# Kernel tuning notes

Hardware: AMD Instinct MI355X
Metric: run time of the kernel (lower is better)

Reference implementation:

```python
import jax, jax.numpy as jnp
import numpy as np

V, BLK, D, H, L = 32000, 2048, 768, 12, 2
HD = D // H

def _ln(x, g, b, eps=1e-5):
    m = jnp.mean(x, axis=-1, keepdims=True)
    v = jnp.var(x, axis=-1, keepdims=True)
    return (x - m) * jax.lax.rsqrt(v + eps) * g + b

def setup_inputs() -> dict:
    key = jax.random.key(0)
    ks = jax.random.split(key, 16)
    s = 0.02
    return {
        "idx": jax.random.randint(ks[0], (2, 2048), 0, V, dtype=jnp.int32),
        "wte": jax.random.normal(ks[1], (V, D), jnp.float32) * s,
        "wpe": jax.random.normal(ks[2], (BLK, D), jnp.float32) * s,
        "ln1_g": jnp.ones((L, D), jnp.float32),
        "ln1_b": jnp.zeros((L, D), jnp.float32),
        "qkv_w": jax.random.normal(ks[3], (L, 3 * D, D), jnp.float32) * s,
        "qkv_b": jnp.zeros((L, 3 * D), jnp.float32),
        "proj_w": jax.random.normal(ks[4], (L, D, D), jnp.float32) * s,
        "proj_b": jnp.zeros((L, D), jnp.float32),
        "ln2_g": jnp.ones((L, D), jnp.float32),
        "ln2_b": jnp.zeros((L, D), jnp.float32),
        "fc_w": jax.random.normal(ks[5], (L, 4 * D, D), jnp.float32) * s,
        "fc_b": jnp.zeros((L, 4 * D), jnp.float32),
        "fc2_w": jax.random.normal(ks[6], (L, D, 4 * D), jnp.float32) * s,
        "fc2_b": jnp.zeros((L, D), jnp.float32),
        "lnf_g": jnp.ones((D,), jnp.float32),
        "lnf_b": jnp.zeros((D,), jnp.float32),
    }

def reference(idx, wte, wpe, ln1_g, ln1_b, qkv_w, qkv_b, proj_w, proj_b,
              ln2_g, ln2_b, fc_w, fc_b, fc2_w, fc2_b, lnf_g, lnf_b):
    B, T = idx.shape
    x = wte[idx] + wpe[:T][None, :, :]  # [B,T,D]
    causal = jnp.tril(jnp.ones((T, T), dtype=bool))
    scale = 1.0 / np.sqrt(HD)
    for l in range(L):
        h = _ln(x, ln1_g[l], ln1_b[l])
        qkv = h @ qkv_w[l].T + qkv_b[l]               # [B,T,3D]
        q, k, v = jnp.split(qkv, 3, axis=-1)
        q = q.reshape(B, T, H, HD).transpose(0, 2, 1, 3)
        k = k.reshape(B, T, H, HD).transpose(0, 2, 1, 3)
        v = v.reshape(B, T, H, HD).transpose(0, 2, 1, 3)
        att = jnp.einsum('bhqd,bhkd->bhqk', q, k) * scale
        att = jnp.where(causal, att, -jnp.inf)
        att = jax.nn.softmax(att, axis=-1)
        y = jnp.einsum('bhqk,bhkd->bhqd', att, v)
        y = y.transpose(0, 2, 1, 3).reshape(B, T, D)
        x = x + y @ proj_w[l].T + proj_b[l]
        h = _ln(x, ln2_g[l], ln2_b[l])
        h = jax.nn.gelu(h @ fc_w[l].T + fc_b[l], approximate=False)
        x = x + h @ fc2_w[l].T + fc2_b[l]
    x = _ln(x, lnf_g, lnf_b)
    logits = x @ wte.T  # tied lm_head, [B,T,V]
    return logits
```

## Files before the change

kernel.cpp:

```cpp
#include <hip/hip_runtime.h>
#include <hip/hip_bf16.h>
#include <math.h>

#define BB 2
#define TT 2048
#define DD 768
#define HH 12
#define NTOK (BB*TT)
#define VV 32000
#define NL 2

typedef __hip_bfloat16 bf16;
typedef __attribute__((ext_vector_type(8))) short bf16x8;
typedef __attribute__((ext_vector_type(4))) float f32x4;

typedef const __attribute__((address_space(1))) unsigned int* gas_u32;
typedef __attribute__((address_space(3))) unsigned int* las_u32;

__device__ __forceinline__ void gload16(const bf16* g, bf16* l) {
    __builtin_amdgcn_global_load_lds((gas_u32)g, (las_u32)l, 16, 0, 0);
}

__global__ void cast_f2b(const float* __restrict__ in, bf16* __restrict__ out, int n4) {
    int i = blockIdx.x * 256 + threadIdx.x;
    if (i >= n4) return;
    float4 v = reinterpret_cast<const float4*>(in)[i];
    out[i*4+0] = __float2bfloat16(v.x);
    out[i*4+1] = __float2bfloat16(v.y);
    out[i*4+2] = __float2bfloat16(v.z);
    out[i*4+3] = __float2bfloat16(v.w);
}

__global__ void embed_k(const int* __restrict__ idx, const float* __restrict__ wte,
                        const float* __restrict__ wpe, float* __restrict__ x) {
    int i = blockIdx.x * 256 + threadIdx.x;
    int n = i / (DD/4), d4 = i - n * (DD/4);
    int tok = idx[n];
    int t = n & (TT - 1);
    float4 a = reinterpret_cast<const float4*>(wte + (size_t)tok * DD)[d4];
    float4 p = reinterpret_cast<const float4*>(wpe + (size_t)t * DD)[d4];
    float4 r; r.x = a.x+p.x; r.y = a.y+p.y; r.z = a.z+p.z; r.w = a.w+p.w;
    reinterpret_cast<float4*>(x)[i] = r;
}

__global__ __launch_bounds__(256) void ln_k(const float* __restrict__ x,
                                            const float* __restrict__ g,
                                            const float* __restrict__ b,
                                            bf16* __restrict__ out) {
    int row = blockIdx.x;
    int tid = threadIdx.x;
    const float* xr = x + (size_t)row * DD;
    float v0 = xr[tid], v1 = xr[tid + 256], v2 = xr[tid + 512];
    float s = v0 + v1 + v2;
    float ss = v0*v0 + v1*v1 + v2*v2;
    #pragma unroll
    for (int d = 1; d < 64; d <<= 1) { s += __shfl_xor(s, d, 64); ss += __shfl_xor(ss, d, 64); }
    __shared__ float sh[8];
    int w = tid >> 6;
    if ((tid & 63) == 0) { sh[w] = s; sh[4 + w] = ss; }
    __syncthreads();
    s  = sh[0] + sh[1] + sh[2] + sh[3];
    ss = sh[4] + sh[5] + sh[6] + sh[7];
    float mean = s * (1.0f / DD);
    float var  = ss * (1.0f / DD) - mean * mean;
    float rstd = rsqrtf(var + 1e-5f);
    bf16* orow = out + (size_t)row * DD;
    orow[tid]       = __float2bfloat16((v0 - mean) * rstd * g[tid]       + b[tid]);
    orow[tid + 256] = __float2bfloat16((v1 - mean) * rstd * g[tid + 256] + b[tid + 256]);
    orow[tid + 512] = __float2bfloat16((v2 - mean) * rstd * g[tid + 512] + b[tid + 512]);
}

template<int EPI>
__global__ __launch_bounds__(256) void gemm_bt(
    const bf16* __restrict__ A, const bf16* __restrict__ W,
    const float* __restrict__ bias, const float* __restrict__ resid,
    void* __restrict__ outp, int O, int K)
{
    __shared__ bf16 As[128 * 32];
    __shared__ bf16 Bs[128 * 32];
    const int tid = threadIdx.x;
    const int lane = tid & 63;
    const int w = tid >> 6;
    const int wm = w >> 1, wn = w & 1;
    const int rowBase = blockIdx.y * 128, colBase = blockIdx.x * 128;

    const int rr = lane & 15, kq = (lane >> 4) * 8;
    const int srow = lane >> 2;
    const int scol = (lane & 3) * 8;

    f32x4 acc[4][4];
    #pragma unroll
    for (int m = 0; m < 4; ++m)
        #pragma unroll
        for (int n = 0; n < 4; ++n) acc[m][n] = (f32x4){0.f, 0.f, 0.f, 0.f};

    for (int k0 = 0; k0 < K; k0 += 32) {
        #pragma unroll
        for (int p = 0; p < 2; ++p) {
            int s = w * 16 + p * 64;
            gload16(&A[(size_t)(rowBase + s + srow) * K + k0 + scol], &As[s * 32]);
            gload16(&W[(size_t)(colBase + s + srow) * K + k0 + scol], &Bs[s * 32]);
        }
        __syncthreads();
        bf16x8 a[4], b[4];
        #pragma unroll
        for (int m = 0; m < 4; ++m)
            a[m] = *reinterpret_cast<const bf16x8*>(&As[(wm * 64 + m * 16 + rr) * 32 + kq]);
        #pragma unroll
        for (int n = 0; n < 4; ++n)
            b[n] = *reinterpret_cast<const bf16x8*>(&Bs[(wn * 64 + n * 16 + rr) * 32 + kq]);
        #pragma unroll
        for (int m = 0; m < 4; ++m)
            #pragma unroll
            for (int n = 0; n < 4; ++n)
                acc[m][n] = __builtin_amdgcn_mfma_f32_16x16x32_bf16(a[m], b[n], acc[m][n], 0, 0, 0);
        __syncthreads();
    }

    #pragma unroll
    for (int m = 0; m < 4; ++m) {
        int row = rowBase + wm * 64 + m * 16 + (lane >> 4) * 4;
        #pragma unroll
        for (int n = 0; n < 4; ++n) {
            int col = colBase + wn * 64 + n * 16 + (lane & 15);
            float bv = bias ? bias[col] : 0.f;
            #pragma unroll
            for (int j2 = 0; j2 < 4; ++j2) {
                float v = acc[m][n][j2] + bv;
                size_t oi = (size_t)(row + j2) * O + col;
                if (EPI == 1) v += resid[oi];
                if (EPI == 2) {
                    v = 0.5f * v * (1.0f + erff(v * 0.70710678118654752f));
                    reinterpret_cast<bf16*>(outp)[oi] = __float2bfloat16(v);
                } else if (EPI == 3) {
                    reinterpret_cast<bf16*>(outp)[oi] = __float2bfloat16(v);
                } else {
                    reinterpret_cast<float*>(outp)[oi] = v;
                }
            }
        }
    }
}

__global__ __launch_bounds__(256) void gemm_lm(
    const bf16* __restrict__ A, const bf16* __restrict__ W,
    float* __restrict__ outp, int O, int K)
{
    __shared__ bf16 As[256 * 32];
    __shared__ bf16 Bs[128 * 32];
    const int tid = threadIdx.x;
    const int lane = tid & 63;
    const int w = tid >> 6;
    const int wm = w >> 1, wn = w & 1;
    const int rowBase = blockIdx.y * 256, colBase = blockIdx.x * 128;

    const int rr = lane & 15, kq = (lane >> 4) * 8;
    const int srow = lane >> 2;
    const int scol = (lane & 3) * 8;

    f32x4 acc[8][4];
    #pragma unroll
    for (int m = 0; m < 8; ++m)
        #pragma unroll
        for (int n = 0; n < 4; ++n) acc[m][n] = (f32x4){0.f, 0.f, 0.f, 0.f};

    for (int k0 = 0; k0 < K; k0 += 32) {
        #pragma unroll
        for (int p = 0; p < 4; ++p) {
            int s = (w + p * 4) * 16;
            gload16(&A[(size_t)(rowBase + s + srow) * K + k0 + scol], &As[s * 32]);
        }
        #pragma unroll
        for (int p = 0; p < 2; ++p) {
            int s = (w + p * 4) * 16;
            gload16(&W[(size_t)(colBase + s + srow) * K + k0 + scol], &Bs[s * 32]);
        }
        __syncthreads();
        bf16x8 b[4];
        #pragma unroll
        for (int n = 0; n < 4; ++n)
            b[n] = *reinterpret_cast<const bf16x8*>(&Bs[(wn * 64 + n * 16 + rr) * 32 + kq]);
        #pragma unroll
        for (int m = 0; m < 8; ++m) {
            bf16x8 a = *reinterpret_cast<const bf16x8*>(&As[(wm * 128 + m * 16 + rr) * 32 + kq]);
            #pragma unroll
            for (int n = 0; n < 4; ++n)
                acc[m][n] = __builtin_amdgcn_mfma_f32_16x16x32_bf16(a, b[n], acc[m][n], 0, 0, 0);
        }
        __syncthreads();
    }

    #pragma unroll
    for (int m = 0; m < 8; ++m) {
        int row = rowBase + wm * 128 + m * 16 + (lane >> 4) * 4;
        #pragma unroll
        for (int n = 0; n < 4; ++n) {
            int col = colBase + wn * 64 + n * 16 + (lane & 15);
            #pragma unroll
            for (int j2 = 0; j2 < 4; ++j2)
                outp[(size_t)(row + j2) * O + col] = acc[m][n][j2];
        }
    }
}

__global__ __launch_bounds__(256, 2) void attn_flash(const bf16* __restrict__ qkvb,
                                                     bf16* __restrict__ ybf)
{
    __shared__ bf16 Qs[128][72];
    __shared__ bf16 Ks[64][72];
    __shared__ bf16 Vt[64][72];

    const int tid = threadIdx.x, lane = tid & 63, w = tid >> 6;
    const int qi = 15 - (blockIdx.x / 24);
    const int bh = blockIdx.x % 24;
    const int b = bh / HH, h = bh % HH;
    const int qbase = qi * 128;
    const int rr = lane & 15, g8 = (lane >> 4) * 8, g4 = (lane >> 4) * 4;

    {
        int seg = tid & 7, jr = tid >> 3;
        #pragma unroll
        for (int p = 0; p < 4; ++p) {
            int q = jr + p * 32;
            *reinterpret_cast<uint4*>(&Qs[q][seg * 8]) =
                *reinterpret_cast<const uint4*>(&qkvb[(size_t)(b*TT + qbase + q) * 2304 + h*64 + seg*8]);
        }
    }
    __syncthreads();

    bf16x8 qf[2][2];
    #pragma unroll
    for (int m = 0; m < 2; ++m)
        #pragma unroll
        for (int c = 0; c < 2; ++c)
            qf[m][c] = *reinterpret_cast<const bf16x8*>(&Qs[w*32 + m*16 + rr][c*32 + g8]);

    float mst[2][4], lst[2][4];
    f32x4 o[2][4];
    #pragma unroll
    for (int m = 0; m < 2; ++m)
        #pragma unroll
        for (int jj = 0; jj < 4; ++jj) { mst[m][jj] = -1e30f; lst[m][jj] = 0.f; }
    #pragma unroll
    for (int m = 0; m < 2; ++m)
        #pragma unroll
        for (int nd = 0; nd < 4; ++nd) o[m][nd] = (f32x4){0.f,0.f,0.f,0.f};

    const int ktmax = 2 * qi + 2;
    for (int kt = 0; kt < ktmax; ++kt) {
        __syncthreads();
        {
            int seg = tid & 7, jr = tid >> 3;
            #pragma unroll
            for (int p = 0; p < 2; ++p) {
                int j = jr + p * 32;
                *reinterpret_cast<uint4*>(&Ks[j][seg * 8]) =
                    *reinterpret_cast<const uint4*>(&qkvb[(size_t)(b*TT + kt*64 + j) * 2304 + DD + h*64 + seg*8]);
            }
            int jv = tid & 31, d0 = (tid >> 5) * 8;
            #pragma unroll
            for (int p = 0; p < 2; ++p) {
                int j = jv + p * 32;
                uint4 raw = *reinterpret_cast<const uint4*>(&qkvb[(size_t)(b*TT + kt*64 + j) * 2304 + 2*DD + h*64 + d0]);
                const bf16* vv = reinterpret_cast<const bf16*>(&raw);
                #pragma unroll
                for (int i2 = 0; i2 < 8; ++i2) Vt[d0 + i2][j] = vv[i2];
            }
        }
        __syncthreads();

        bf16x8 kf[4][2];
        #pragma unroll
        for (int n = 0; n < 4; ++n)
            #pragma unroll
            for (int c = 0; c < 2; ++c)
                kf[n][c] = *reinterpret_cast<const bf16x8*>(&Ks[n*16 + rr][c*32 + g8]);
        f32x4 sacc[2][4];
        #pragma unroll
        for (int m = 0; m < 2; ++m)
            #pragma unroll
            for (int n = 0; n < 4; ++n) sacc[m][n] = (f32x4){0.f,0.f,0.f,0.f};
        #pragma unroll
        for (int m = 0; m < 2; ++m)
            #pragma unroll
            for (int n = 0; n < 4; ++n)
                #pragma unroll
                for (int c = 0; c < 2; ++c)
                    sacc[m][n] = __builtin_amdgcn_mfma_f32_16x16x32_bf16(qf[m][c], kf[n][c], sacc[m][n], 0, 0, 0);

        float corr[2][4];
        #pragma unroll
        for (int m = 0; m < 2; ++m) {
            #pragma unroll
            for (int jj = 0; jj < 4; ++jj) {
                const int qg = qbase + w*32 + m*16 + g4 + jj;
                float pm = -1e30f;
                #pragma unroll
                for (int n = 0; n < 4; ++n) {
                    float v = sacc[m][n][jj] * 0.125f;
                    int jg = kt*64 + n*16 + rr;
                    v = (jg <= qg) ? v : -1e30f;
                    sacc[m][n][jj] = v;
                    pm = fmaxf(pm, v);
                }
                pm = fmaxf(pm, __shfl_xor(pm, 1, 64));
                pm = fmaxf(pm, __shfl_xor(pm, 2, 64));
                pm = fmaxf(pm, __shfl_xor(pm, 4, 64));
                pm = fmaxf(pm, __shfl_xor(pm, 8, 64));
                float nm = fmaxf(mst[m][jj], pm);
                float cv = __expf(mst[m][jj] - nm);
                float r = 0.f;
                #pragma unroll
                for (int n = 0; n < 4; ++n) {
                    float p = __expf(sacc[m][n][jj] - nm);
                    r += p;
                    Qs[w*32 + m*16 + g4 + jj][n*16 + rr] = __float2bfloat16(p);
                }
                r += __shfl_xor(r, 1, 64);
                r += __shfl_xor(r, 2, 64);
                r += __shfl_xor(r, 4, 64);
                r += __shfl_xor(r, 8, 64);
                lst[m][jj] = lst[m][jj] * cv + r;
                mst[m][jj] = nm;
                corr[m][jj] = cv;
            }
        }
        #pragma unroll
        for (int m = 0; m < 2; ++m)
            #pragma unroll
            for (int nd = 0; nd < 4; ++nd)
                #pragma unroll
                for (int jj = 0; jj < 4; ++jj) o[m][nd][jj] *= corr[m][jj];

        __builtin_amdgcn_sched_barrier(0);

        bf16x8 pf[2][2], vf[4][2];
        #pragma unroll
        for (int m = 0; m < 2; ++m)
            #pragma unroll
            for (int c = 0; c < 2; ++c)
                pf[m][c] = *reinterpret_cast<const bf16x8*>(&Qs[w*32 + m*16 + rr][c*32 + g8]);
        #pragma unroll
        for (int nd = 0; nd < 4; ++nd)
            #pragma unroll
            for (int c = 0; c < 2; ++c)
                vf[nd][c] = *reinterpret_cast<const bf16x8*>(&Vt[nd*16 + rr][c*32 + g8]);
        #pragma unroll
        for (int m = 0; m < 2; ++m)
            #pragma unroll
            for (int nd = 0; nd < 4; ++nd)
                #pragma unroll
                for (int c = 0; c < 2; ++c)
                    o[m][nd] = __builtin_amdgcn_mfma_f32_16x16x32_bf16(pf[m][c], vf[nd][c], o[m][nd], 0, 0, 0);
    }

    #pragma unroll
    for (int m = 0; m < 2; ++m) {
        #pragma unroll
        for (int jj = 0; jj < 4; ++jj) {
            const int qg = qbase + w*32 + m*16 + g4 + jj;
            const float inv = 1.0f / lst[m][jj];
            #pragma unroll
            for (int nd = 0; nd < 4; ++nd)
                ybf[(size_t)(b*TT + qg) * DD + h*64 + nd*16 + rr] =
                    __float2bfloat16(o[m][nd][jj] * inv);
        }
    }
}

extern "C" void kernel_launch(void* const* d_in, const int* in_sizes, int n_in,
                              void* d_out, int out_size, void* d_ws, size_t ws_size,
                              hipStream_t stream) {
    const int*   idx    = (const int*)  d_in[0];
    const float* wte    = (const float*)d_in[1];
    const float* wpe    = (const float*)d_in[2];
    const float* ln1_g  = (const float*)d_in[3];
    const float* ln1_b  = (const float*)d_in[4];
    const float* qkv_w  = (const float*)d_in[5];
    const float* qkv_b  = (const float*)d_in[6];
    const float* proj_w = (const float*)d_in[7];
    const float* proj_b = (const float*)d_in[8];
    const float* ln2_g  = (const float*)d_in[9];
    const float* ln2_b  = (const float*)d_in[10];
    const float* fc_w   = (const float*)d_in[11];
    const float* fc_b   = (const float*)d_in[12];
    const float* fc2_w  = (const float*)d_in[13];
    const float* fc2_b  = (const float*)d_in[14];
    const float* lnf_g  = (const float*)d_in[15];
    const float* lnf_b  = (const float*)d_in[16];

    char* ws = (char*)d_ws;
    size_t off = 0;
    auto alloc = [&](size_t bytes) -> void* {
        void* p = ws + off;
        off += (bytes + 255) & ~(size_t)255;
        return p;
    };
    float* x     = (float*)alloc((size_t)NTOK * DD * 4);
    bf16*  qkvb  = (bf16*) alloc((size_t)NTOK * 3 * DD * 2);
    bf16*  lnb   = (bf16*) alloc((size_t)NTOK * DD * 2);
    bf16*  ybf   = (bf16*) alloc((size_t)NTOK * DD * 2);
    bf16*  ffb   = (bf16*) alloc((size_t)NTOK * 4 * DD * 2);
    bf16*  w_qkv = (bf16*) alloc((size_t)NL * 3 * DD * DD * 2);
    bf16*  w_prj = (bf16*) alloc((size_t)NL * DD * DD * 2);
    bf16*  w_fc  = (bf16*) alloc((size_t)NL * 4 * DD * DD * 2);
    bf16*  w_fc2 = (bf16*) alloc((size_t)NL * DD * 4 * DD * 2);
    bf16*  w_wte = (bf16*) alloc((size_t)VV * DD * 2);

    auto conv = [&](const float* src, bf16* dst, size_t n) {
        int n4 = (int)(n / 4);
        cast_f2b<<<dim3((n4 + 255) / 256), dim3(256), 0, stream>>>(src, dst, n4);
    };
    conv(wte,    w_wte, (size_t)VV * DD);
    conv(qkv_w,  w_qkv, (size_t)NL * 3 * DD * DD);
    conv(proj_w, w_prj, (size_t)NL * DD * DD);
    conv(fc_w,   w_fc,  (size_t)NL * 4 * DD * DD);
    conv(fc2_w,  w_fc2, (size_t)NL * DD * 4 * DD);

    embed_k<<<dim3(NTOK * (DD/4) / 256), dim3(256), 0, stream>>>(idx, wte, wpe, x);

    for (int l = 0; l < NL; ++l) {
        ln_k<<<dim3(NTOK), dim3(256), 0, stream>>>(x, ln1_g + l * DD, ln1_b + l * DD, lnb);
        gemm_bt<3><<<dim3(3 * DD / 128, 32), dim3(256), 0, stream>>>(
            lnb, w_qkv + (size_t)l * 3 * DD * DD, qkv_b + l * 3 * DD, nullptr,
            (void*)qkvb, 3 * DD, DD);
        attn_flash<<<dim3(24 * (TT / 128)), dim3(256), 0, stream>>>(qkvb, ybf);
        gemm_bt<1><<<dim3(DD / 128, 32), dim3(256), 0, stream>>>(
            ybf, w_prj + (size_t)l * DD * DD, proj_b + l * DD, x,
            (void*)x, DD, DD);
        ln_k<<<dim3(NTOK), dim3(256), 0, stream>>>(x, ln2_g + l * DD, ln2_b + l * DD, lnb);
        gemm_bt<2><<<dim3(4 * DD / 128, 32), dim3(256), 0, stream>>>(
            lnb, w_fc + (size_t)l * 4 * DD * DD, fc_b + l * 4 * DD, nullptr,
            (void*)ffb, 4 * DD, DD);
        gemm_bt<1><<<dim3(DD / 128, 32), dim3(256), 0, stream>>>(
            ffb, w_fc2 + (size_t)l * DD * 4 * DD, fc2_b + l * DD, x,
            (void*)x, DD, 4 * DD);
    }

    ln_k<<<dim3(NTOK), dim3(256), 0, stream>>>(x, lnf_g, lnf_b, lnb);
    gemm_lm<<<dim3(VV / 128, NTOK / 256), dim3(256), 0, stream>>>(
        lnb, w_wte, (float*)d_out, VV, DD);
}
```

Measured before the change: 915.4 us.

## Add pipelined 256x256 GEMM kernel for QKV, FC and LM head

```diff
diff --git a/kernel.cpp b/kernel.cpp
--- a/kernel.cpp
+++ b/kernel.cpp
@@ -71,6 +71,105 @@
 }
 
 template<int EPI>
+__global__ __launch_bounds__(512, 1) void gemm256(
+    const bf16* __restrict__ A, const bf16* __restrict__ W,
+    const float* __restrict__ bias, const float* __restrict__ resid,
+    void* __restrict__ outp, int O, int K)
+{
+    __shared__ bf16 smem_bf[65536];
+    char* smem = (char*)smem_bf;
+    const int tid = threadIdx.x, lane = tid & 63, wid = tid >> 6;
+    const int wm = wid >> 2, wn = wid & 3;
+    const int rowBase = blockIdx.y * 256, colBase = blockIdx.x * 256;
+    const int rr = lane & 15, s4 = lane >> 4;
+    const int swz = (rr >> 1) & 3;
+    const int aOff = (wm * 128 + rr) * 64 + ((s4 ^ swz) << 4);
+    const int bOff = (wn * 64 + rr) * 64 + ((s4 ^ swz) << 4);
+    const int st_r = (wid << 4) + (lane >> 2);
+    const int st_j = lane & 3;
+    const bf16* Asrc = A + (size_t)rowBase * K;
+    const bf16* Wsrc = W + (size_t)colBase * K;
+    const int nk = K >> 6;
+
+    auto STAGE = [&](const bf16* src, int mat, int kt, int kk) {
+        char* base = smem + ((kt & 1) << 16) + (mat << 15) + (kk << 14);
+        #pragma unroll
+        for (int L = 0; L < 2; ++L) {
+            int r = (L << 7) + st_r;
+            int gs = st_j ^ ((r >> 1) & 3);
+            gload16(src + (size_t)r * K + (kt << 6) + (kk << 5) + (gs << 3),
+                    (bf16*)(base + (L << 13) + (wid << 10)));
+        }
+    };
+
+    f32x4 acc[8][4];
+    #pragma unroll
+    for (int m = 0; m < 8; ++m)
+        #pragma unroll
+        for (int n = 0; n < 4; ++n) acc[m][n] = (f32x4){0.f, 0.f, 0.f, 0.f};
+
+    STAGE(Asrc, 0, 0, 0); STAGE(Wsrc, 1, 0, 0); STAGE(Asrc, 0, 0, 1); STAGE(Wsrc, 1, 0, 1);
+    STAGE(Asrc, 0, 1, 0); STAGE(Wsrc, 1, 1, 0); STAGE(Asrc, 0, 1, 1);
+    asm volatile("s_waitcnt vmcnt(6)" ::: "memory");
+    __builtin_amdgcn_s_barrier();
+
+    bf16x8 af[8], bfr[2];
+    for (int kt = 0; kt < nk; ++kt) {
+        char* Ab = smem + ((kt & 1) << 16);
+        char* Bb = Ab + 32768;
+        #pragma unroll
+        for (int q = 0; q < 4; ++q) {
+            const int kk = q >> 1, nh = q & 1;
+            if (nh == 0) {
+                #pragma unroll
+                for (int m = 0; m < 8; ++m)
+                    af[m] = *reinterpret_cast<const bf16x8*>(Ab + (kk << 14) + aOff + (m << 10));
+            }
+            bfr[0] = *reinterpret_cast<const bf16x8*>(Bb + (kk << 14) + bOff + ((nh * 2 + 0) << 10));
+            bfr[1] = *reinterpret_cast<const bf16x8*>(Bb + (kk << 14) + bOff + ((nh * 2 + 1) << 10));
+            if (q == 0) { if (kt + 1 < nk) STAGE(Wsrc, 1, kt + 1, 1); }
+            else if (q == 1) { if (kt + 2 < nk) STAGE(Asrc, 0, kt + 2, 0); }
+            else if (q == 2) { if (kt + 2 < nk) STAGE(Wsrc, 1, kt + 2, 0); }
+            else { if (kt + 2 < nk) STAGE(Asrc, 0, kt + 2, 1); }
+            __builtin_amdgcn_s_barrier();
+            __builtin_amdgcn_s_setprio(1);
+            #pragma unroll
+            for (int m = 0; m < 8; ++m) {
+                acc[m][nh * 2 + 0] = __builtin_amdgcn_mfma_f32_16x16x32_bf16(af[m], bfr[0], acc[m][nh * 2 + 0], 0, 0, 0);
+                acc[m][nh * 2 + 1] = __builtin_amdgcn_mfma_f32_16x16x32_bf16(af[m], bfr[1], acc[m][nh * 2 + 1], 0, 0, 0);
+            }
+            __builtin_amdgcn_s_setprio(0);
+            if (q == 3) asm volatile("s_waitcnt vmcnt(6)" ::: "memory");
+            __builtin_amdgcn_s_barrier();
+        }
+    }
+
+    #pragma unroll
+    for (int m = 0; m < 8; ++m) {
+        int row = rowBase + wm * 128 + m * 16 + s4 * 4;
+        #pragma unroll
+        for (int n = 0; n < 4; ++n) {
+            int col = colBase + wn * 64 + n * 16 + rr;
+            float bv = bias ? bias[col] : 0.f;
+            #pragma unroll
+            for (int j2 = 0; j2 < 4; ++j2) {
+                float v = acc[m][n][j2] + bv;
+                size_t oi = (size_t)(row + j2) * O + col;
+                if (EPI == 1) v += resid[oi];
+                if (EPI == 2) {
+                    v = 0.5f * v * (1.0f + erff(v * 0.70710678118654752f));
+                    reinterpret_cast<bf16*>(outp)[oi] = __float2bfloat16(v);
+                } else if (EPI == 3) {
+                    reinterpret_cast<bf16*>(outp)[oi] = __float2bfloat16(v);
+                } else {
+                    reinterpret_cast<float*>(outp)[oi] = v;
+                }
+            }
+        }
+    }
+}
+
+template<int EPI>
 __global__ __launch_bounds__(256) void gemm_bt(
     const bf16* __restrict__ A, const bf16* __restrict__ W,
     const float* __restrict__ bias, const float* __restrict__ resid,
@@ -129,76 +228,8 @@
                 float v = acc[m][n][j2] + bv;
                 size_t oi = (size_t)(row + j2) * O + col;
                 if (EPI == 1) v += resid[oi];
-                if (EPI == 2) {
-                    v = 0.5f * v * (1.0f + erff(v * 0.70710678118654752f));
-                    reinterpret_cast<bf16*>(outp)[oi] = __float2bfloat16(v);
-                } else if (EPI == 3) {
-                    reinterpret_cast<bf16*>(outp)[oi] = __float2bfloat16(v);
-                } else {
-                    reinterpret_cast<float*>(outp)[oi] = v;
-                }
-            }
-        }
-    }
-}
-
-__global__ __launch_bounds__(256) void gemm_lm(
-    const bf16* __restrict__ A, const bf16* __restrict__ W,
-    float* __restrict__ outp, int O, int K)
-{
-    __shared__ bf16 As[256 * 32];
-    __shared__ bf16 Bs[128 * 32];
-    const int tid = threadIdx.x;
-    const int lane = tid & 63;
-    const int w = tid >> 6;
-    const int wm = w >> 1, wn = w & 1;
-    const int rowBase = blockIdx.y * 256, colBase = blockIdx.x * 128;
-
-    const int rr = lane & 15, kq = (lane >> 4) * 8;
-    const int srow = lane >> 2;
-    const int scol = (lane & 3) * 8;
-
-    f32x4 acc[8][4];
-    #pragma unroll
-    for (int m = 0; m < 8; ++m)
-        #pragma unroll
-        for (int n = 0; n < 4; ++n) acc[m][n] = (f32x4){0.f, 0.f, 0.f, 0.f};
-
-    for (int k0 = 0; k0 < K; k0 += 32) {
-        #pragma unroll
-        for (int p = 0; p < 4; ++p) {
-            int s = (w + p * 4) * 16;
-            gload16(&A[(size_t)(rowBase + s + srow) * K + k0 + scol], &As[s * 32]);
-        }
-        #pragma unroll
-        for (int p = 0; p < 2; ++p) {
-            int s = (w + p * 4) * 16;
-            gload16(&W[(size_t)(colBase + s + srow) * K + k0 + scol], &Bs[s * 32]);
-        }
-        __syncthreads();
-        bf16x8 b[4];
-        #pragma unroll
-        for (int n = 0; n < 4; ++n)
-            b[n] = *reinterpret_cast<const bf16x8*>(&Bs[(wn * 64 + n * 16 + rr) * 32 + kq]);
-        #pragma unroll
-        for (int m = 0; m < 8; ++m) {
-            bf16x8 a = *reinterpret_cast<const bf16x8*>(&As[(wm * 128 + m * 16 + rr) * 32 + kq]);
-            #pragma unroll
-            for (int n = 0; n < 4; ++n)
-                acc[m][n] = __builtin_amdgcn_mfma_f32_16x16x32_bf16(a, b[n], acc[m][n], 0, 0, 0);
-        }
-        __syncthreads();
-    }
-
-    #pragma unroll
-    for (int m = 0; m < 8; ++m) {
-        int row = rowBase + wm * 128 + m * 16 + (lane >> 4) * 4;
-        #pragma unroll
-        for (int n = 0; n < 4; ++n) {
-            int col = colBase + wn * 64 + n * 16 + (lane & 15);
-            #pragma unroll
-            for (int j2 = 0; j2 < 4; ++j2)
-                outp[(size_t)(row + j2) * O + col] = acc[m][n][j2];
+                reinterpret_cast<float*>(outp)[oi] = v;
+            }
         }
     }
 }
@@ -421,7 +452,7 @@
 
     for (int l = 0; l < NL; ++l) {
         ln_k<<<dim3(NTOK), dim3(256), 0, stream>>>(x, ln1_g + l * DD, ln1_b + l * DD, lnb);
-        gemm_bt<3><<<dim3(3 * DD / 128, 32), dim3(256), 0, stream>>>(
+        gemm256<3><<<dim3(3 * DD / 256, NTOK / 256), dim3(512), 0, stream>>>(
             lnb, w_qkv + (size_t)l * 3 * DD * DD, qkv_b + l * 3 * DD, nullptr,
             (void*)qkvb, 3 * DD, DD);
         attn_flash<<<dim3(24 * (TT / 128)), dim3(256), 0, stream>>>(qkvb, ybf);
@@ -429,7 +460,7 @@
             ybf, w_prj + (size_t)l * DD * DD, proj_b + l * DD, x,
             (void*)x, DD, DD);
         ln_k<<<dim3(NTOK), dim3(256), 0, stream>>>(x, ln2_g + l * DD, ln2_b + l * DD, lnb);
-        gemm_bt<2><<<dim3(4 * DD / 128, 32), dim3(256), 0, stream>>>(
+        gemm256<2><<<dim3(4 * DD / 256, NTOK / 256), dim3(512), 0, stream>>>(
             lnb, w_fc + (size_t)l * 4 * DD * DD, fc_b + l * 4 * DD, nullptr,
             (void*)ffb, 4 * DD, DD);
         gemm_bt<1><<<dim3(DD / 128, 32), dim3(256), 0, stream>>>(
@@ -438,6 +469,6 @@
     }
 
     ln_k<<<dim3(NTOK), dim3(256), 0, stream>>>(x, lnf_g, lnf_b, lnb);
-    gemm_lm<<<dim3(VV / 128, NTOK / 256), dim3(256), 0, stream>>>(
-        lnb, w_wte, (float*)d_out, VV, DD);
-}
+    gemm256<0><<<dim3(VV / 256, NTOK / 256), dim3(512), 0, stream>>>(
+        lnb, w_wte, nullptr, nullptr, d_out, VV, DD);
+}
```

Result: slower. 957.8 us (+4.6%).
